# Optimization experiments

Hardware: AMD Instinct MI355X
Metric: run time of the kernel (lower is better)

The kernel has to match this reference:

```python
import jax, jax.numpy as jnp
import numpy as np

B, T, D, F = 4, 2048, 2048, 8192
RANK = 16
ALPHA = 32.0
SCALING = ALPHA / RANK  # rslora=False -> alpha/rank = 2.0


def setup_inputs() -> dict:
    key = jax.random.key(0)
    k_x, k_w, k_a, k_b = jax.random.split(key, 4)
    x = jax.random.normal(k_x, (B, T, D), dtype=jnp.float32)
    # Main weight: real init_fn default is zeros; use randn for a meaningful baseline.
    w = jax.random.normal(k_w, (D, F), dtype=jnp.float32) * 0.02
    # LoRA factors: config.init_fn = normal(stddev=0.01)
    lora_a = jax.random.normal(k_a, (D, RANK), dtype=jnp.float32) * 0.01
    lora_b = jax.random.normal(k_b, (RANK, F), dtype=jnp.float32) * 0.01
    return {"x": x, "w": w, "lora_a": lora_a, "lora_b": lora_b}


def reference(x, w, lora_a, lora_b):
    # eqn:   btd,df->btf   (main GEMM)
    # eqn_a: btd,dL->btL   (LoRA down-projection, L = rank)
    # eqn_b: btL,Lf->btf   (LoRA up-projection)
    result = jnp.einsum('btd,df->btf', x, w.astype(x.dtype))
    lora = jnp.einsum('btd,dL->btL', x, lora_a.astype(x.dtype))
    lora = jnp.einsum('btL,Lf->btf', lora, lora_b.astype(x.dtype))
    return result + lora * SCALING
```

## Files before the change

### kernel.cpp

```cpp
#include <hip/hip_runtime.h>
#include <stdint.h>
#include <stddef.h>


typedef __bf16 bf16;
typedef __bf16 bf16x4 __attribute__((ext_vector_type(4)));
typedef __bf16 bf16x8 __attribute__((ext_vector_type(8)));
typedef float  f32x4  __attribute__((ext_vector_type(4)));

#define M_DIM 8192
#define N_DIM 8192
#define K_DIM 2048
#define LRANK 16
#define LSCALE 2.0f

#define BM 128
#define BN 128
#define BK 64

typedef __attribute__((address_space(1))) void* as1_void;
typedef __attribute__((address_space(3))) void* as3_void;

__device__ __forceinline__ void gload_lds16(const void* g, void* l) {
    __builtin_amdgcn_global_load_lds((as1_void)(g), (as3_void)(l), 16, 0, 0);
}

__global__ void convert_x_kernel(const float* __restrict__ x,
                                 bf16* __restrict__ xb) {
    int i = (blockIdx.x * blockDim.x + threadIdx.x) * 4;
    float4 v = *(const float4*)(x + i);
    bf16x4 o;
    o.x = (bf16)v.x; o.y = (bf16)v.y; o.z = (bf16)v.z; o.w = (bf16)v.w;
    *(bf16x4*)(xb + i) = o;
}

__global__ void fold_transpose_kernel(const float* __restrict__ w,
                                      const float* __restrict__ la,
                                      const float* __restrict__ lb,
                                      bf16* __restrict__ wt) {
    __shared__ float tile[32][33];
    __shared__ float at[32][17];
    __shared__ float bt[16][32];

    const int k0 = blockIdx.x * 32;
    const int n0 = blockIdx.y * 32;
    const int t  = threadIdx.x;
    const int c  = t & 31;
    const int r0 = t >> 5;

    #pragma unroll
    for (int rr = 0; rr < 32; rr += 8)
        tile[r0 + rr][c] = w[(size_t)(k0 + r0 + rr) * N_DIM + n0 + c];

    at[t >> 4][t & 15]          = la[(size_t)(k0 + (t >> 4)) * LRANK + (t & 15)];
    at[(t + 256) >> 4][t & 15]  = la[(size_t)(k0 + ((t + 256) >> 4)) * LRANK + (t & 15)];

    bt[t >> 5][c]       = lb[(size_t)(t >> 5) * N_DIM + n0 + c];
    bt[(t >> 5) + 8][c] = lb[(size_t)((t >> 5) + 8) * N_DIM + n0 + c];

    __syncthreads();

    #pragma unroll
    for (int rr = 0; rr < 32; rr += 8) {
        const int nl = r0 + rr;
        const int kl = c;
        float delta = 0.f;
        #pragma unroll
        for (int L = 0; L < LRANK; ++L)
            delta += at[kl][L] * bt[L][nl];
        float v = tile[kl][nl] + LSCALE * delta;
        wt[(size_t)(n0 + nl) * K_DIM + k0 + kl] = (bf16)v;
    }
}

__global__ __launch_bounds__(256)
void gemm_bf16_kernel(const bf16* __restrict__ A,
                      const bf16* __restrict__ Bt,
                      float* __restrict__ C) {
    __shared__ __align__(16) bf16 As[BM * BK];
    __shared__ __align__(16) bf16 Bs[BN * BK];

    const int t    = threadIdx.x;
    const int lane = t & 63;
    const int wave = t >> 6;
    const int wm   = (wave >> 1) * 64;
    const int wn   = (wave & 1) * 64;

    const int n0 = blockIdx.x * BN;
    const int m0 = blockIdx.y * BM;

    int rowS[4], clS[4];
    #pragma unroll
    for (int j = 0; j < 4; ++j) {
        int p   = j * 4096 + t * 16;
        int row = p >> 7;
        int cp  = (p >> 4) & 7;
        rowS[j] = row;
        clS[j]  = cp ^ (row & 7);
    }
    const bf16* aBase = A  + (size_t)m0 * K_DIM;
    const bf16* bBase = Bt + (size_t)n0 * K_DIM;

    int offA[2][4], offB[2][4];
    #pragma unroll
    for (int ks = 0; ks < 2; ++ks) {
        #pragma unroll
        for (int i = 0; i < 4; ++i) {
            int rowa = wm + i * 16 + (lane & 15);
            int rowb = wn + i * 16 + (lane & 15);
            int cl   = ks * 4 + (lane >> 4);
            offA[ks][i] = rowa * 64 + ((cl ^ (rowa & 7)) * 8);
            offB[ks][i] = rowb * 64 + ((cl ^ (rowb & 7)) * 8);
        }
    }

    f32x4 acc[4][4] = {};

    for (int kt = 0; kt < K_DIM / BK; ++kt) {
        const int k0 = kt * BK;
        #pragma unroll
        for (int j = 0; j < 4; ++j) {
            gload_lds16(aBase + (size_t)rowS[j] * K_DIM + k0 + clS[j] * 8,
                        As + j * 2048 + t * 8);
            gload_lds16(bBase + (size_t)rowS[j] * K_DIM + k0 + clS[j] * 8,
                        Bs + j * 2048 + t * 8);
        }
        __syncthreads();

        #pragma unroll
        for (int ks = 0; ks < 2; ++ks) {
            bf16x8 af[4], bfr[4];
            #pragma unroll
            for (int i = 0; i < 4; ++i) af[i]  = *(const bf16x8*)(As + offA[ks][i]);
            #pragma unroll
            for (int i = 0; i < 4; ++i) bfr[i] = *(const bf16x8*)(Bs + offB[ks][i]);
            #pragma unroll
            for (int mi = 0; mi < 4; ++mi)
                #pragma unroll
                for (int ni = 0; ni < 4; ++ni)
                    acc[mi][ni] = __builtin_amdgcn_mfma_f32_16x16x32_bf16(
                        af[mi], bfr[ni], acc[mi][ni], 0, 0, 0);
        }
        __syncthreads();
    }

    const int cr = (lane >> 4) * 4;
    const int cc = lane & 15;
    float* cBase = C + (size_t)(m0 + wm + cr) * N_DIM + (n0 + wn + cc);
    #pragma unroll
    for (int mi = 0; mi < 4; ++mi)
        #pragma unroll
        for (int r = 0; r < 4; ++r)
            #pragma unroll
            for (int ni = 0; ni < 4; ++ni)
                cBase[(size_t)(mi * 16 + r) * N_DIM + ni * 16] = acc[mi][ni][r];
}

extern "C" void kernel_launch(void* const* d_in, const int* in_sizes, int n_in,
                              void* d_out, int out_size, void* d_ws, size_t ws_size,
                              hipStream_t stream) {
    const float* x  = (const float*)d_in[0];
    const float* w  = (const float*)d_in[1];
    const float* la = (const float*)d_in[2];
    const float* lb = (const float*)d_in[3];
    float* out = (float*)d_out;

    bf16* xb = (bf16*)d_ws;
    bf16* wt = (bf16*)((char*)d_ws + (size_t)M_DIM * K_DIM * 2);

    convert_x_kernel<<<M_DIM * K_DIM / 4 / 256, 256, 0, stream>>>(x, xb);
    fold_transpose_kernel<<<dim3(K_DIM / 32, N_DIM / 32), 256, 0, stream>>>(w, la, lb, wt);
    gemm_bf16_kernel<<<dim3(N_DIM / BN, M_DIM / BM), 256, 0, stream>>>(xb, wt, out);
}
```

Measured before the change: 622.7 us.

## Rewrite GEMM as 256x256 double-buffered 8-wave pipeline with priority scheduling

Replaces the 128x128 single-buffered GEMM with a 256x256 tile using 512 threads and double-buffered LDS. Global-to-LDS loads for the next k-tiles are interleaved with MFMA quadrants, using manual vmcnt/lgkmcnt waits, barriers, and s_setprio. It also adds an XCD-aware block-id swizzle. The aim is to hide memory latency and raise data reuse per tile, at the cost of 128KB of LDS and heavy register use with two blocks per CU.

```diff
diff --git a/kernel.cpp b/kernel.cpp
--- a/kernel.cpp
+++ b/kernel.cpp
@@ -14,9 +14,10 @@
 #define LRANK 16
 #define LSCALE 2.0f
 
-#define BM 128
-#define BN 128
+#define BM 256
+#define BN 256
 #define BK 64
+#define NT (K_DIM / BK)
 
 typedef __attribute__((address_space(1))) void* as1_void;
 typedef __attribute__((address_space(3))) void* as3_void;
@@ -73,87 +74,150 @@
     }
 }
 
-__global__ __launch_bounds__(256)
+
+#define BAR()   __builtin_amdgcn_s_barrier()
+#define WAITL() do { asm volatile("s_waitcnt lgkmcnt(0)" ::: "memory"); \
+                     __builtin_amdgcn_sched_barrier(0); } while (0)
+#define WAITV4() asm volatile("s_waitcnt vmcnt(4)" ::: "memory")
+#define PRHI()  __builtin_amdgcn_s_setprio(1)
+#define PRLO()  __builtin_amdgcn_s_setprio(0)
+
+#define STAGE_A(t, h, buf) do {                                                   \
+    _Pragma("unroll")                                                             \
+    for (int c_ = 0; c_ < 2; ++c_)                                                \
+        gload_lds16(aG + (size_t)((h) * 128 + prow[c_]) * K_DIM + (t) * BK + pcl[c_] * 8, \
+                    As + (buf) * (BM * BK) + (h) * 8192 + c_ * 4096 + tid * 8);   \
+} while (0)
+
+#define STAGE_B(t, h, buf) do {                                                   \
+    _Pragma("unroll")                                                             \
+    for (int c_ = 0; c_ < 2; ++c_)                                                \
+        gload_lds16(bG + (size_t)((h) * 128 + prow[c_]) * K_DIM + (t) * BK + pcl[c_] * 8, \
+                    Bs + (buf) * (BN * BK) + (h) * 8192 + c_ * 4096 + tid * 8);   \
+} while (0)
+
+#define RD_A(grp, buf) do {                                                       \
+    _Pragma("unroll")                                                             \
+    for (int q_ = 0; q_ < 4; ++q_) {                                              \
+        af[q_][0] = *(const bf16x8*)(As + (buf) * (BM * BK) + baseA[(grp) + q_]); \
+        af[q_][1] = *(const bf16x8*)(As + (buf) * (BM * BK) + (baseA[(grp) + q_] ^ 32)); \
+    }                                                                             \
+} while (0)
+
+#define RD_B(dst, jlo, buf) do {                                                  \
+    _Pragma("unroll")                                                             \
+    for (int q_ = 0; q_ < 2; ++q_) {                                              \
+        dst[q_][0] = *(const bf16x8*)(Bs + (buf) * (BN * BK) + baseB[(jlo) + q_]);\
+        dst[q_][1] = *(const bf16x8*)(Bs + (buf) * (BN * BK) + (baseB[(jlo) + q_] ^ 32)); \
+    }                                                                             \
+} while (0)
+
+#define MMQ(I0, J0, BF) do {                                                      \
+    _Pragma("unroll")                                                             \
+    for (int q_ = 0; q_ < 4; ++q_)                                                \
+        _Pragma("unroll")                                                         \
+        for (int jj_ = 0; jj_ < 2; ++jj_)                                         \
+            _Pragma("unroll")                                                     \
+            for (int ks_ = 0; ks_ < 2; ++ks_)                                     \
+                acc[(I0) + q_][(J0) + jj_] = __builtin_amdgcn_mfma_f32_16x16x32_bf16( \
+                    af[q_][ks_], BF[jj_][ks_], acc[(I0) + q_][(J0) + jj_], 0, 0, 0);  \
+} while (0)
+
+__global__ __launch_bounds__(512, 2)
 void gemm_bf16_kernel(const bf16* __restrict__ A,
                       const bf16* __restrict__ Bt,
                       float* __restrict__ C) {
-    __shared__ __align__(16) bf16 As[BM * BK];
-    __shared__ __align__(16) bf16 Bs[BN * BK];
-
-    const int t    = threadIdx.x;
-    const int lane = t & 63;
-    const int wave = t >> 6;
-    const int wm   = (wave >> 1) * 64;
-    const int wn   = (wave & 1) * 64;
-
-    const int n0 = blockIdx.x * BN;
-    const int m0 = blockIdx.y * BM;
-
-    int rowS[4], clS[4];
+    __shared__ __align__(16) bf16 As[2 * BM * BK];
+    __shared__ __align__(16) bf16 Bs[2 * BN * BK];
+
+    const int tid  = threadIdx.x;
+    const int lane = tid & 63;
+    const int wave = tid >> 6;
+    const int wm   = (wave >> 2) * 64;
+    const int wn   = (wave & 3) * 32;
+
+    const int id  = blockIdx.y * 32 + blockIdx.x;
+    const int swz = (id & 7) * 128 + (id >> 3);
+    const int m0  = (swz >> 5) * BM;
+    const int n0  = (swz & 31) * BN;
+
+    int prow[2], pcl[2];
+    #pragma unroll
+    for (int c = 0; c < 2; ++c) {
+        int p   = c * 8192 + tid * 16;
+        prow[c] = p >> 7;
+        pcl[c]  = ((p >> 4) & 7) ^ (prow[c] & 7);
+    }
+    const bf16* aG = A  + (size_t)m0 * K_DIM;
+    const bf16* bG = Bt + (size_t)n0 * K_DIM;
+
+    int baseA[8], baseB[4];
+    #pragma unroll
+    for (int i = 0; i < 8; ++i) {
+        int ra = ((i & 4) ? 128 : 0) + wm + (i & 3) * 16 + (lane & 15);
+        baseA[i] = ra * 64 + (((lane >> 4) ^ (ra & 7)) * 8);
+    }
     #pragma unroll
     for (int j = 0; j < 4; ++j) {
-        int p   = j * 4096 + t * 16;
-        int row = p >> 7;
-        int cp  = (p >> 4) & 7;
-        rowS[j] = row;
-        clS[j]  = cp ^ (row & 7);
-    }
-    const bf16* aBase = A  + (size_t)m0 * K_DIM;
-    const bf16* bBase = Bt + (size_t)n0 * K_DIM;
-
-    int offA[2][4], offB[2][4];
-    #pragma unroll
-    for (int ks = 0; ks < 2; ++ks) {
-        #pragma unroll
-        for (int i = 0; i < 4; ++i) {
-            int rowa = wm + i * 16 + (lane & 15);
-            int rowb = wn + i * 16 + (lane & 15);
-            int cl   = ks * 4 + (lane >> 4);
-            offA[ks][i] = rowa * 64 + ((cl ^ (rowa & 7)) * 8);
-            offB[ks][i] = rowb * 64 + ((cl ^ (rowb & 7)) * 8);
-        }
-    }
-
-    f32x4 acc[4][4] = {};
-
-    for (int kt = 0; kt < K_DIM / BK; ++kt) {
-        const int k0 = kt * BK;
+        int rb = ((j & 2) ? 128 : 0) + wn + (j & 1) * 16 + (lane & 15);
+        baseB[j] = rb * 64 + (((lane >> 4) ^ (rb & 7)) * 8);
+    }
+
+    f32x4 acc[8][4] = {};
+    bf16x8 af[4][2], bA[2][2], bBv[2][2];
+
+    STAGE_A(0, 0, 0); STAGE_B(0, 0, 0);
+    STAGE_A(0, 1, 0); STAGE_B(0, 1, 0);
+    STAGE_A(1, 0, 1); STAGE_B(1, 0, 1);
+    WAITV4();
+    BAR();
+
+    for (int it = 0; it < NT / 2; ++it) {
+        const int t1 = 2 * it + 1;
+        const int t2 = (2 * it + 2 < NT) ? 2 * it + 2 : NT - 1;
+        const int t3 = (2 * it + 3 < NT) ? 2 * it + 3 : NT - 1;
+
+        RD_A(0, 0); RD_B(bA, 0, 0);
+        STAGE_A(t1, 1, 1);
+        BAR(); WAITL(); PRHI(); MMQ(0, 0, bA); PRLO(); BAR();
+        RD_B(bBv, 2, 0);
+        STAGE_B(t1, 1, 1);
+        BAR(); WAITL(); PRHI(); MMQ(0, 2, bBv); PRLO(); BAR();
+        RD_A(4, 0);
+        STAGE_A(t2, 0, 0);
+        BAR(); WAITL(); PRHI(); MMQ(4, 0, bA); PRLO(); BAR();
+        STAGE_B(t2, 0, 0);
+        WAITV4();
+        BAR(); PRHI(); MMQ(4, 2, bBv); PRLO(); BAR();
+
+        RD_A(0, 1); RD_B(bA, 0, 1);
+        STAGE_A(t2, 1, 0);
+        BAR(); WAITL(); PRHI(); MMQ(0, 0, bA); PRLO(); BAR();
+        RD_B(bBv, 2, 1);
+        STAGE_B(t2, 1, 0);
+        BAR(); WAITL(); PRHI(); MMQ(0, 2, bBv); PRLO(); BAR();
+        RD_A(4, 1);
+        STAGE_A(t3, 0, 1);
+        BAR(); WAITL(); PRHI(); MMQ(4, 0, bA); PRLO(); BAR();
+        STAGE_B(t3, 0, 1);
+        WAITV4();
+        BAR(); PRHI(); MMQ(4, 2, bBv); PRLO(); BAR();
+    }
+
+    const int cr = (lane >> 4) * 4;
+    const int cc = lane & 15;
+    #pragma unroll
+    for (int i = 0; i < 8; ++i) {
+        const int row = m0 + ((i & 4) ? 128 : 0) + wm + (i & 3) * 16 + cr;
         #pragma unroll
         for (int j = 0; j < 4; ++j) {
-            gload_lds16(aBase + (size_t)rowS[j] * K_DIM + k0 + clS[j] * 8,
-                        As + j * 2048 + t * 8);
-            gload_lds16(bBase + (size_t)rowS[j] * K_DIM + k0 + clS[j] * 8,
-                        Bs + j * 2048 + t * 8);
+            const int col = n0 + ((j & 2) ? 128 : 0) + wn + (j & 1) * 16 + cc;
+            float* cp = C + (size_t)row * N_DIM + col;
+            #pragma unroll
+            for (int r = 0; r < 4; ++r)
+                cp[(size_t)r * N_DIM] = acc[i][j][r];
         }
-        __syncthreads();
-
-        #pragma unroll
-        for (int ks = 0; ks < 2; ++ks) {
-            bf16x8 af[4], bfr[4];
-            #pragma unroll
-            for (int i = 0; i < 4; ++i) af[i]  = *(const bf16x8*)(As + offA[ks][i]);
-            #pragma unroll
-            for (int i = 0; i < 4; ++i) bfr[i] = *(const bf16x8*)(Bs + offB[ks][i]);
-            #pragma unroll
-            for (int mi = 0; mi < 4; ++mi)
-                #pragma unroll
-                for (int ni = 0; ni < 4; ++ni)
-                    acc[mi][ni] = __builtin_amdgcn_mfma_f32_16x16x32_bf16(
-                        af[mi], bfr[ni], acc[mi][ni], 0, 0, 0);
-        }
-        __syncthreads();
-    }
-
-    const int cr = (lane >> 4) * 4;
-    const int cc = lane & 15;
-    float* cBase = C + (size_t)(m0 + wm + cr) * N_DIM + (n0 + wn + cc);
-    #pragma unroll
-    for (int mi = 0; mi < 4; ++mi)
-        #pragma unroll
-        for (int r = 0; r < 4; ++r)
-            #pragma unroll
-            for (int ni = 0; ni < 4; ++ni)
-                cBase[(size_t)(mi * 16 + r) * N_DIM + ni * 16] = acc[mi][ni][r];
+    }
 }
 
 extern "C" void kernel_launch(void* const* d_in, const int* in_sizes, int n_in,
@@ -170,5 +234,5 @@
 
     convert_x_kernel<<<M_DIM * K_DIM / 4 / 256, 256, 0, stream>>>(x, xb);
     fold_transpose_kernel<<<dim3(K_DIM / 32, N_DIM / 32), 256, 0, stream>>>(w, la, lb, wt);
-    gemm_bf16_kernel<<<dim3(N_DIM / BN, M_DIM / BM), 256, 0, stream>>>(xb, wt, out);
-}
+    gemm_bf16_kernel<<<dim3(N_DIM / BN, M_DIM / BM), 512, 0, stream>>>(xb, wt, out);
+}
```

New measurement: 603.3 us. 3.1% less time.
